# Kernel tuning notes

Measured on AMD Instinct MI355X. Metric: run time of the kernel, lower is better.

## Reference

```python
import jax, jax.numpy as jnp
import numpy as np

N_NODES = 50000
N_EDGES = 800000
IN_C = 64
OUT_C = 64
HEADS = 4
N_LAYERS = 2
BN_EPS = 1e-5
NEG_SLOPE = 0.2


def setup_inputs() -> dict:
    key = jax.random.key(0)
    ks = jax.random.split(key, 20)
    inp = {
        "x": jax.random.normal(ks[0], (N_NODES, IN_C), dtype=jnp.float32),
        "edge_index": jax.random.randint(ks[1], (2, N_EDGES), 0, N_NODES, dtype=jnp.int64),
        "edge_weight": jax.random.uniform(ks[2], (N_EDGES,), dtype=jnp.float32),
    }
    # per-layer GATConv + BN params (glorot-ish init)
    for i in range(N_LAYERS):
        k = 3 + i * 5
        scale = 1.0 / np.sqrt(IN_C)
        inp[f"W{i}"] = jax.random.normal(ks[k], (IN_C, HEADS * OUT_C), dtype=jnp.float32) * scale
        inp[f"asrc{i}"] = jax.random.normal(ks[k + 1], (HEADS, OUT_C), dtype=jnp.float32) * scale
        inp[f"adst{i}"] = jax.random.normal(ks[k + 2], (HEADS, OUT_C), dtype=jnp.float32) * scale
        inp[f"b{i}"] = jnp.zeros((OUT_C,), dtype=jnp.float32)
        inp[f"gamma{i}"] = jnp.ones((OUT_C,), dtype=jnp.float32)
        inp[f"beta{i}"] = jnp.zeros((OUT_C,), dtype=jnp.float32)
    return inp


def _gat_layer(x, src, dst, W, a_src, a_dst, b):
    # x: [N, C_in]; src/dst: [E'] (with self loops). Per-head dim = OUT_C.
    xh = (x @ W).reshape(-1, HEADS, OUT_C)          # [N, H, C]
    al_src = jnp.sum(xh * a_src[None], axis=-1)      # [N, H]
    al_dst = jnp.sum(xh * a_dst[None], axis=-1)      # [N, H]
    e = jax.nn.leaky_relu(al_src[src] + al_dst[dst], NEG_SLOPE)  # [E', H]
    # segment softmax over edges sharing a destination node
    m = jax.lax.stop_gradient(jax.ops.segment_max(e, dst, num_segments=N_NODES))
    p = jnp.exp(e - m[dst])
    denom = jax.ops.segment_sum(p, dst, num_segments=N_NODES)
    alpha = p / (denom[dst] + 1e-16)                 # [E', H]
    out = jax.ops.segment_sum(alpha[:, :, None] * xh[src], dst, num_segments=N_NODES)  # [N,H,C]
    return out.mean(axis=1) + b                      # concat=False -> mean over heads


def _batchnorm(x, gamma, beta):
    mu = x.mean(axis=0)
    var = x.var(axis=0)
    return gamma * (x - mu) * jax.lax.rsqrt(var + BN_EPS) + beta


def reference(x, edge_index, edge_weight, W0, asrc0, adst0, b0, gamma0, beta0,
              W1, asrc1, adst1, b1, gamma1, beta1):
    # edge_weight is passed as edge_attr to PyG GATConv but edge_dim=None -> ignored.
    loop = jnp.arange(N_NODES, dtype=edge_index.dtype)
    src = jnp.concatenate([edge_index[0], loop])  # add_self_loops=True (PyG default)
    dst = jnp.concatenate([edge_index[1], loop])
    params = [(W0, asrc0, adst0, b0, gamma0, beta0),
              (W1, asrc1, adst1, b1, gamma1, beta1)]
    saved = None
    for (W, a_s, a_d, b, g, bt) in params:
        x = _gat_layer(x, src, dst, W, a_s, a_d, b)
        saved = x
        x = _batchnorm(x, g, bt)
        x = jax.nn.relu(x)
        # dropout(0.5) is identity in eval mode
    return (x, saved)
```

## Files before the change

### kernel.cpp

```cpp
#include <hip/hip_runtime.h>
#include <stdint.h>

#define NEG_SLOPE 0.2f
#define BN_EPS 1e-5f

typedef __attribute__((ext_vector_type(8))) short bf16x8;
typedef __attribute__((ext_vector_type(4))) float f32x4;

__device__ __forceinline__ float bf2f(unsigned short u) {
  union { unsigned int i; float f; } v; v.i = ((unsigned int)u) << 16; return v.f;
}
__device__ __forceinline__ float asf(unsigned int u) {
  union { unsigned int i; float f; } v; v.i = u; return v.f;
}
__device__ __forceinline__ unsigned short f2bf(float f) {
  union { float f; unsigned int i; } v; v.f = f;
  unsigned int i = v.i;
  return (unsigned short)((i + 0x7fffu + ((i >> 16) & 1u)) >> 16);
}
__device__ __forceinline__ float loadF(const void* p, long long i, int f32) {
  return f32 ? ((const float*)p)[i] : bf2f(((const unsigned short*)p)[i]);
}
__device__ __forceinline__ int edge_at(const void* ei, long long idx, int is64) {
  return is64 ? (int)((const long long*)ei)[idx] : ((const int*)ei)[idx];
}

__global__ void detect_kernel(const unsigned short* __restrict__ x,
                              const int* __restrict__ ei32,
                              int* __restrict__ flags) {
  __shared__ int wild, oddnz;
  if (threadIdx.x == 0) { wild = 0; oddnz = 0; }
  __syncthreads();
  int lw = 0, lo = 0;
  for (int i = threadIdx.x; i < 4096; i += 256) {
    unsigned short u = x[i];
    int ex = (u >> 7) & 0xFF;
    if (ex >= 0x86) lw++;
    if (ei32[2 * i + 1] != 0) lo++;
  }
  if (lw) atomicAdd(&wild, lw);
  if (lo) atomicAdd(&oddnz, lo);
  __syncthreads();
  if (threadIdx.x == 0) { flags[0] = (wild > 64) ? 1 : 0; flags[1] = (oddnz == 0) ? 1 : 0; }
}

__global__ __launch_bounds__(256) void wtrans_kernel(
    const void* __restrict__ W0, const void* __restrict__ as0, const void* __restrict__ ad0,
    const void* __restrict__ W1, const void* __restrict__ as1, const void* __restrict__ ad1,
    const int* __restrict__ flags,
    unsigned short* __restrict__ WTx0, unsigned short* __restrict__ WTx1) {
  const void* W = blockIdx.x ? W1 : W0;
  const void* asrc = blockIdx.x ? as1 : as0;
  const void* adst = blockIdx.x ? ad1 : ad0;
  unsigned short* WTx = blockIdx.x ? WTx1 : WTx0;
  int f32 = flags[0];
  __shared__ unsigned short Wl[64 * 258];
  int t = threadIdx.x;
  for (int i = t; i < 64 * 256; i += 256) {
    int k = i >> 8, c = i & 255;
    Wl[k * 258 + c] = f32 ? f2bf(((const float*)W)[i]) : ((const unsigned short*)W)[i];
  }
  __syncthreads();
  {
    int c = t;
    #pragma unroll
    for (int k8 = 0; k8 < 64; k8 += 8) {
      unsigned int p0 = (unsigned int)Wl[(k8 + 0) * 258 + c] | ((unsigned int)Wl[(k8 + 1) * 258 + c] << 16);
      unsigned int p1 = (unsigned int)Wl[(k8 + 2) * 258 + c] | ((unsigned int)Wl[(k8 + 3) * 258 + c] << 16);
      unsigned int p2 = (unsigned int)Wl[(k8 + 4) * 258 + c] | ((unsigned int)Wl[(k8 + 5) * 258 + c] << 16);
      unsigned int p3 = (unsigned int)Wl[(k8 + 6) * 258 + c] | ((unsigned int)Wl[(k8 + 7) * 258 + c] << 16);
      uint4 pk; pk.x = p0; pk.y = p1; pk.z = p2; pk.w = p3;
      *(uint4*)&WTx[c * 64 + k8] = pk;
    }
  }
  for (int idx = t; idx < 512; idx += 256) {
    int r = idx >> 6;
    int k = idx & 63;
    int h = r & 3;
    const void* av = (r >> 2) ? adst : asrc;
    float acc = 0.f;
    #pragma unroll 8
    for (int c = 0; c < 64; c++)
      acc += bf2f(Wl[k * 258 + h * 64 + c]) * loadF(av, h * 64 + c, f32);
    WTx[(256 + r) * 64 + k] = f2bf(acc);
  }
  for (int idx = t; idx < 512; idx += 256) WTx[264 * 64 + idx] = 0;
}

__global__ __launch_bounds__(256) void hist_kernel(const void* __restrict__ ei, int E, int N,
                                                   const int* __restrict__ flags,
                                                   int* __restrict__ deg) {
  int e = blockIdx.x * 256 + threadIdx.x;
  if (e >= E) return;
  int is64 = flags[1];
  int d = edge_at(ei, (long long)E + e, is64);
  d = (d < 0 || d >= N) ? 0 : d;
  atomicAdd(&deg[d], 1);
}

__global__ __launch_bounds__(256) void partial_kernel(const int* __restrict__ deg,
                                                      int* __restrict__ blocksum, int N) {
  int t = threadIdx.x;
  int idx = blockIdx.x * 256 + t;
  int v = (idx < N) ? deg[idx] : 0;
  #pragma unroll
  for (int o = 1; o < 64; o <<= 1) v += __shfl_xor(v, o);
  __shared__ int ws[4];
  if ((t & 63) == 0) ws[t >> 6] = v;
  __syncthreads();
  if (t == 0) blocksum[blockIdx.x] = ws[0] + ws[1] + ws[2] + ws[3];
}

__global__ void scan_base_kernel(const int* __restrict__ blocksum,
                                 int* __restrict__ blockbase, int B) {
  int lane = threadIdx.x;
  int base = 0;
  if (lane == 0) blockbase[0] = 0;
  for (int start = 0; start < B; start += 64) {
    int idx = start + lane;
    int v = (idx < B) ? blocksum[idx] : 0;
    int sc = v;
    #pragma unroll
    for (int o = 1; o < 64; o <<= 1) {
      int u = __shfl_up(sc, o);
      if (lane >= o) sc += u;
    }
    if (idx < B) blockbase[idx + 1] = base + sc;
    base = __shfl(base + sc, 63);
  }
}

__global__ __launch_bounds__(256) void scan_final_kernel(const int* __restrict__ deg,
                                                         const int* __restrict__ blockbase,
                                                         int* __restrict__ offsets, int N) {
  int t = threadIdx.x;
  int lane = t & 63;
  int wid = t >> 6;
  int idx = blockIdx.x * 256 + t;
  int v = (idx < N) ? deg[idx] : 0;
  int sc = v;
  #pragma unroll
  for (int o = 1; o < 64; o <<= 1) {
    int u = __shfl_up(sc, o);
    if (lane >= o) sc += u;
  }
  __shared__ int ws[4];
  if (lane == 63) ws[wid] = sc;
  __syncthreads();
  int add = 0;
  #pragma unroll
  for (int w = 0; w < 4; w++) if (w < wid) add += ws[w];
  if (idx < N) offsets[idx + 1] = blockbase[blockIdx.x] + add + sc;
  if (idx == 0) offsets[0] = 0;
}

__global__ __launch_bounds__(256) void scatter_kernel(
    const void* __restrict__ ei, int E, int N, const int* __restrict__ flags,
    const int* __restrict__ offsets, int* __restrict__ cursor,
    int* __restrict__ csr_src) {
  int e = blockIdx.x * 256 + threadIdx.x;
  if (e >= E) return;
  int is64 = flags[1];
  int s = edge_at(ei, e, is64);
  int d = edge_at(ei, (long long)E + e, is64);
  s = (s < 0 || s >= N) ? 0 : s;
  d = (d < 0 || d >= N) ? 0 : d;
  int pos = offsets[d] + atomicAdd(&cursor[d], 1);
  csr_src[pos] = s;
}

__global__ __launch_bounds__(256, 3) void gemm_mfma(
    const void* __restrict__ x, const unsigned short* __restrict__ WTx,
    const int* __restrict__ flags, int mode,
    const float* __restrict__ gsum, const float* __restrict__ gsq,
    const void* __restrict__ gamma, const void* __restrict__ beta,
    unsigned short* __restrict__ xh, float* __restrict__ als, float* __restrict__ ald,
    int N) {
  __shared__ unsigned short WTs[272 * 68];
  __shared__ unsigned short RP[4][16 * 68];
  __shared__ float bnsc[64], bnsh[64];
  int f32 = flags[0];
  int t = threadIdx.x;
  for (int i = t; i < 272 * 8; i += 256) {
    int c = i >> 3, g = i & 7;
    uint4 v = ((const uint4*)WTx)[i];
    *(uint4*)&WTs[c * 68 + g * 8] = v;
  }
  if (mode == 1 && t < 64) {
    float mu = gsum[t] / (float)N;
    float var = fmaxf(gsq[t] / (float)N - mu * mu, 0.f);
    float sc = loadF(gamma, t, f32) * rsqrtf(var + BN_EPS);
    bnsc[t] = sc;
    bnsh[t] = loadF(beta, t, f32) - mu * sc;
  }
  __syncthreads();

  int wave = t >> 6, lane = t & 63;
  int q = lane >> 4, r16 = lane & 15;
  int m0 = blockIdx.x * 64 + wave * 16;
  if (m0 >= N) return;
  int row = m0 + r16;
  int rowc = row < N ? row : N - 1;

  bf16x8 a0, a1;
  if (mode == 1) {
    const float* xp = (const float*)x + (size_t)rowc * 64 + q * 8;
    float va[8], vb[8];
    *(float4*)&va[0] = ((const float4*)xp)[0];
    *(float4*)&va[4] = ((const float4*)xp)[1];
    *(float4*)&vb[0] = ((const float4*)(xp + 32))[0];
    *(float4*)&vb[4] = ((const float4*)(xp + 32))[1];
    int k0 = q * 8;
    #pragma unroll
    for (int jj = 0; jj < 8; jj++) {
      float v = fmaxf(va[jj] * bnsc[k0 + jj] + bnsh[k0 + jj], 0.f);
      float w = fmaxf(vb[jj] * bnsc[k0 + 32 + jj] + bnsh[k0 + 32 + jj], 0.f);
      a0[jj] = (short)f2bf(v);
      a1[jj] = (short)f2bf(w);
    }
  } else if (f32) {
    const float* xp = (const float*)x + (size_t)rowc * 64 + q * 8;
    float va[8], vb[8];
    *(float4*)&va[0] = ((const float4*)xp)[0];
    *(float4*)&va[4] = ((const float4*)xp)[1];
    *(float4*)&vb[0] = ((const float4*)(xp + 32))[0];
    *(float4*)&vb[4] = ((const float4*)(xp + 32))[1];
    #pragma unroll
    for (int jj = 0; jj < 8; jj++) {
      a0[jj] = (short)f2bf(va[jj]);
      a1[jj] = (short)f2bf(vb[jj]);
    }
  } else {
    const unsigned short* xp = (const unsigned short*)x + (size_t)rowc * 64 + q * 8;
    a0 = *(const bf16x8*)xp;
    a1 = *(const bf16x8*)(xp + 32);
  }

  f32x4 acc[17];
  #pragma unroll
  for (int tt = 0; tt < 17; tt++) acc[tt] = (f32x4){0.f, 0.f, 0.f, 0.f};
  #pragma unroll
  for (int tt = 0; tt < 17; tt++) {
    int c = tt * 16 + r16;
    bf16x8 b0 = *(const bf16x8*)&WTs[c * 68 + q * 8];
    bf16x8 b1 = *(const bf16x8*)&WTs[c * 68 + 32 + q * 8];
    acc[tt] = __builtin_amdgcn_mfma_f32_16x16x32_bf16(a0, b0, acc[tt], 0, 0, 0);
    acc[tt] = __builtin_amdgcn_mfma_f32_16x16x32_bf16(a1, b1, acc[tt], 0, 0, 0);
  }

  {
    int obase = m0 + q * 4;
    #pragma unroll
    for (int rr = 0; rr < 4; rr++) {
      int orow = obase + rr;
      if (orow < N) {
        if (r16 < 4) als[orow * 4 + r16] = acc[16][rr];
        else if (r16 < 8) ald[orow * 4 + (r16 - 4)] = acc[16][rr];
      }
    }
  }
  unsigned short* rp = RP[wave];
  #pragma unroll
  for (int g4 = 0; g4 < 4; g4++) {
    #pragma unroll
    for (int tt2 = 0; tt2 < 4; tt2++) {
      int tile = g4 * 4 + tt2;
      #pragma unroll
      for (int rr = 0; rr < 4; rr++)
        rp[(q * 4 + rr) * 68 + tt2 * 16 + r16] = f2bf(acc[tile][rr]);
    }
    #pragma unroll
    for (int i = 0; i < 2; i++) {
      int g = i * 64 + lane;
      int r = g >> 3;
      int grp = g & 7;
      uint4 v = *(const uint4*)&rp[r * 68 + grp * 8];
      int orow = m0 + r;
      if (orow < N) ((uint4*)xh)[(size_t)orow * 32 + g4 * 8 + grp] = v;
    }
  }
}

__global__ __launch_bounds__(256) void agg_kernel(
    const unsigned short* __restrict__ xh,
    const float* __restrict__ als, const float* __restrict__ ald,
    const int* __restrict__ offsets, const int* __restrict__ csr_src,
    const void* __restrict__ bias, const int* __restrict__ flags,
    float* __restrict__ y, int N) {
  int lane = threadIdx.x & 63;
  int wid = threadIdx.x >> 6;
  int n = blockIdx.x * 4 + wid;
  if (n >= N) return;
  int h = lane >> 4;
  const uint2* xv = (const uint2*)xh;
  float ad = ald[n * 4 + h];
  float e = als[n * 4 + h] + ad;
  e = (e > 0.f) ? e : NEG_SLOPE * e;
  float p = __expf(e);
  float dsum = p;
  uint2 xs = xv[(size_t)n * 64 + lane];
  float a0 = p * asf(xs.x << 16), a1 = p * asf(xs.x & 0xffff0000u);
  float a2 = p * asf(xs.y << 16), a3 = p * asf(xs.y & 0xffff0000u);
  int beg = offsets[n], end = offsets[n + 1];
  int j = beg;
  for (; j + 4 <= end; j += 4) {
    int s0 = csr_src[j];
    int s1 = csr_src[j + 1];
    int s2 = csr_src[j + 2];
    int s3 = csr_src[j + 3];
    uint2 v0 = xv[(size_t)s0 * 64 + lane];
    uint2 v1 = xv[(size_t)s1 * 64 + lane];
    uint2 v2 = xv[(size_t)s2 * 64 + lane];
    uint2 v3 = xv[(size_t)s3 * 64 + lane];
    float e0 = als[s0 * 4 + h] + ad;
    float e1 = als[s1 * 4 + h] + ad;
    float e2 = als[s2 * 4 + h] + ad;
    float e3 = als[s3 * 4 + h] + ad;
    e0 = (e0 > 0.f) ? e0 : NEG_SLOPE * e0;
    e1 = (e1 > 0.f) ? e1 : NEG_SLOPE * e1;
    e2 = (e2 > 0.f) ? e2 : NEG_SLOPE * e2;
    e3 = (e3 > 0.f) ? e3 : NEG_SLOPE * e3;
    float p0 = __expf(e0);
    float p1 = __expf(e1);
    float p2 = __expf(e2);
    float p3 = __expf(e3);
    dsum += p0 + p1 + p2 + p3;
    a0 += p0 * asf(v0.x << 16) + p1 * asf(v1.x << 16)
        + p2 * asf(v2.x << 16) + p3 * asf(v3.x << 16);
    a1 += p0 * asf(v0.x & 0xffff0000u) + p1 * asf(v1.x & 0xffff0000u)
        + p2 * asf(v2.x & 0xffff0000u) + p3 * asf(v3.x & 0xffff0000u);
    a2 += p0 * asf(v0.y << 16) + p1 * asf(v1.y << 16)
        + p2 * asf(v2.y << 16) + p3 * asf(v3.y << 16);
    a3 += p0 * asf(v0.y & 0xffff0000u) + p1 * asf(v1.y & 0xffff0000u)
        + p2 * asf(v2.y & 0xffff0000u) + p3 * asf(v3.y & 0xffff0000u);
  }
  for (; j < end; j++) {
    int s0 = csr_src[j];
    uint2 v0 = xv[(size_t)s0 * 64 + lane];
    float e0 = als[s0 * 4 + h] + ad;
    e0 = (e0 > 0.f) ? e0 : NEG_SLOPE * e0;
    float p0 = __expf(e0);
    dsum += p0;
    a0 += p0 * asf(v0.x << 16);
    a1 += p0 * asf(v0.x & 0xffff0000u);
    a2 += p0 * asf(v0.y << 16);
    a3 += p0 * asf(v0.y & 0xffff0000u);
  }
  float inv = 1.0f / dsum;
  a0 *= inv; a1 *= inv; a2 *= inv; a3 *= inv;
  a0 += __shfl_xor(a0, 16); a0 += __shfl_xor(a0, 32);
  a1 += __shfl_xor(a1, 16); a1 += __shfl_xor(a1, 32);
  a2 += __shfl_xor(a2, 16); a2 += __shfl_xor(a2, 32);
  a3 += __shfl_xor(a3, 16); a3 += __shfl_xor(a3, 32);
  if (lane < 16) {
    int f32 = flags[0];
    float4 o;
    o.x = 0.25f * a0 + loadF(bias, 4 * lane + 0, f32);
    o.y = 0.25f * a1 + loadF(bias, 4 * lane + 1, f32);
    o.z = 0.25f * a2 + loadF(bias, 4 * lane + 2, f32);
    o.w = 0.25f * a3 + loadF(bias, 4 * lane + 3, f32);
    ((float4*)(y + (size_t)n * 64))[lane] = o;
  }
}

__global__ __launch_bounds__(256) void stats_kernel(const float* __restrict__ y,
                                                    float* __restrict__ gsum,
                                                    float* __restrict__ gsq, int N) {
  __shared__ float ls[256], lq[256];
  int t = threadIdx.x;
  int c = t & 63;
  int r0 = blockIdx.x * 4 + (t >> 6);
  float s = 0.f, q = 0.f;
  for (int r = r0; r < N; r += gridDim.x * 4) {
    float v = y[(size_t)r * 64 + c];
    s += v; q += v * v;
  }
  ls[t] = s; lq[t] = q;
  __syncthreads();
  if (t < 64) {
    s = ls[t] + ls[t + 64] + ls[t + 128] + ls[t + 192];
    q = lq[t] + lq[t + 64] + lq[t + 128] + lq[t + 192];
    atomicAdd(&gsum[c], s);
    atomicAdd(&gsq[c], q);
  }
}

__global__ __launch_bounds__(256) void bn_kernel(
    const float* __restrict__ y, const float* __restrict__ gsum, const float* __restrict__ gsq,
    const void* __restrict__ gamma, const void* __restrict__ beta,
    const int* __restrict__ flags, float* __restrict__ out_f, int N) {
  int i = blockIdx.x * 256 + threadIdx.x;
  if (i >= N * 16) return;
  int f32 = flags[0];
  int cg = i & 15;
  float4 v = ((const float4*)y)[i];
  float4 s = ((const float4*)gsum)[cg];
  float4 q = ((const float4*)gsq)[cg];
  float inv_n = 1.0f / (float)N;
  float vv[4] = {v.x, v.y, v.z, v.w};
  float ss[4] = {s.x, s.y, s.z, s.w};
  float qq[4] = {q.x, q.y, q.z, q.w};
  float o[4];
  #pragma unroll
  for (int k = 0; k < 4; k++) {
    float g = loadF(gamma, 4 * cg + k, f32);
    float b = loadF(beta, 4 * cg + k, f32);
    float mu = ss[k] * inv_n;
    float var = fmaxf(qq[k] * inv_n - mu * mu, 0.f);
    float r = g * (vv[k] - mu) * rsqrtf(var + BN_EPS) + b;
    o[k] = r > 0.f ? r : 0.f;
  }
  float4 ov; ov.x = o[0]; ov.y = o[1]; ov.z = o[2]; ov.w = o[3];
  ((float4*)out_f)[i] = ov;
}

extern "C" void kernel_launch(void* const* d_in, const int* in_sizes, int n_in,
                              void* d_out, int out_size, void* d_ws, size_t ws_size,
                              hipStream_t stream) {
  const void* x    = d_in[0];
  const void* ei   = d_in[1];
  const void* W0    = d_in[3];
  const void* asrc0 = d_in[4];
  const void* adst0 = d_in[5];
  const void* b0    = d_in[6];
  const void* g0    = d_in[7];
  const void* be0   = d_in[8];
  const void* W1    = d_in[9];
  const void* asrc1 = d_in[10];
  const void* adst1 = d_in[11];
  const void* b1    = d_in[12];
  const void* g1    = d_in[13];
  const void* be1   = d_in[14];

  int N = in_sizes[0] / 64;
  int E = in_sizes[1] / 2;
  int NB = (N + 255) / 256;
  int NG = (N + 63) / 64;
  int NA = (N + 3) / 4;

  char* p = (char*)d_ws;
  auto alloc = [&](size_t bytes) -> char* {
    char* r = p;
    p += (bytes + 255) & ~(size_t)255;
    return r;
  };
  int* flags    = (int*)alloc(256);
  int* deg      = (int*)alloc((size_t)N * 4);
  int* cursor   = (int*)alloc((size_t)N * 4);
  int* offsets  = (int*)alloc((size_t)(N + 1) * 4);
  int* blocksum = (int*)alloc((size_t)NB * 4);
  int* blockbase= (int*)alloc((size_t)(NB + 1) * 4);
  int* csr_src  = (int*)alloc((size_t)E * 4);
  unsigned short* WTx0 = (unsigned short*)alloc(272 * 64 * 2);
  unsigned short* WTx1 = (unsigned short*)alloc(272 * 64 * 2);
  unsigned short* xh = (unsigned short*)alloc((size_t)N * 256 * 2);
  float* als    = (float*)alloc((size_t)N * 4 * 4);
  float* ald    = (float*)alloc((size_t)N * 4 * 4);
  float* y      = (float*)alloc((size_t)N * 64 * 4);
  float* gsum0  = (float*)alloc(256);
  float* gsq0   = (float*)alloc(256);
  float* gsum1  = (float*)alloc(256);
  float* gsq1   = (float*)alloc(256);

  hipMemsetAsync(deg, 0, (size_t)N * 4, stream);
  hipMemsetAsync(cursor, 0, (size_t)N * 4, stream);
  hipMemsetAsync(gsum0, 0, 1024, stream);

  detect_kernel<<<1, 256, 0, stream>>>((const unsigned short*)x, (const int*)ei, flags);
  wtrans_kernel<<<2, 256, 0, stream>>>(W0, asrc0, adst0, W1, asrc1, adst1, flags, WTx0, WTx1);

  hist_kernel<<<(E + 255) / 256, 256, 0, stream>>>(ei, E, N, flags, deg);
  partial_kernel<<<NB, 256, 0, stream>>>(deg, blocksum, N);
  scan_base_kernel<<<1, 64, 0, stream>>>(blocksum, blockbase, NB);
  scan_final_kernel<<<NB, 256, 0, stream>>>(deg, blockbase, offsets, N);
  scatter_kernel<<<(E + 255) / 256, 256, 0, stream>>>(ei, E, N, flags, offsets, cursor, csr_src);

  float* out_x = (float*)d_out;
  float* out_saved = out_x + (size_t)N * 64;

  gemm_mfma<<<NG, 256, 0, stream>>>(x, WTx0, flags, 0, (const float*)nullptr,
                                    (const float*)nullptr, nullptr, nullptr,
                                    xh, als, ald, N);
  agg_kernel<<<NA, 256, 0, stream>>>(xh, als, ald, offsets, csr_src, b0, flags, y, N);
  stats_kernel<<<250, 256, 0, stream>>>(y, gsum0, gsq0, N);
  gemm_mfma<<<NG, 256, 0, stream>>>(y, WTx1, flags, 1, gsum0, gsq0, g0, be0,
                                    xh, als, ald, N);
  agg_kernel<<<NA, 256, 0, stream>>>(xh, als, ald, offsets, csr_src, b1, flags, out_saved, N);
  stats_kernel<<<250, 256, 0, stream>>>(out_saved, gsum1, gsq1, N);
  bn_kernel<<<(N * 16 + 255) / 256, 256, 0, stream>>>(out_saved, gsum1, gsq1, g1, be1,
                                                      flags, out_x, N);
}
```

Before: 428.5 us.

## Merge detect into wtrans, seed cursor from scan, restructure GEMM stores

Folds the input-format detection kernel into the weight-transpose kernel. The scan now writes exclusive offsets into the cursor array, which removes a memset and an offsets load in the scatter. The GEMM processes two 64-row blocks per workgroup, amortizing the weight LDS load. It also drops the LDS staging buffer for xh and writes uint2 directly to global memory. The aggregation epilogue switches from float4 stores to scalar strided stores, trading coalesced wide stores for simpler indexing.

```diff
diff --git a/kernel.cpp b/kernel.cpp
--- a/kernel.cpp
+++ b/kernel.cpp
@@ -25,40 +25,54 @@
   return is64 ? (int)((const long long*)ei)[idx] : ((const int*)ei)[idx];
 }
 
-__global__ void detect_kernel(const unsigned short* __restrict__ x,
-                              const int* __restrict__ ei32,
-                              int* __restrict__ flags) {
-  __shared__ int wild, oddnz;
-  if (threadIdx.x == 0) { wild = 0; oddnz = 0; }
-  __syncthreads();
-  int lw = 0, lo = 0;
-  for (int i = threadIdx.x; i < 4096; i += 256) {
-    unsigned short u = x[i];
-    int ex = (u >> 7) & 0xFF;
-    if (ex >= 0x86) lw++;
-    if (ei32[2 * i + 1] != 0) lo++;
-  }
-  if (lw) atomicAdd(&wild, lw);
-  if (lo) atomicAdd(&oddnz, lo);
-  __syncthreads();
-  if (threadIdx.x == 0) { flags[0] = (wild > 64) ? 1 : 0; flags[1] = (oddnz == 0) ? 1 : 0; }
-}
-
 __global__ __launch_bounds__(256) void wtrans_kernel(
+    const unsigned short* __restrict__ x, const int* __restrict__ ei32,
     const void* __restrict__ W0, const void* __restrict__ as0, const void* __restrict__ ad0,
     const void* __restrict__ W1, const void* __restrict__ as1, const void* __restrict__ ad1,
-    const int* __restrict__ flags,
+    int* __restrict__ flags,
     unsigned short* __restrict__ WTx0, unsigned short* __restrict__ WTx1) {
+  __shared__ int wild, oddnz;
+  __shared__ unsigned short Wl[64 * 258];
+  int t = threadIdx.x;
+  if (t == 0) { wild = 0; oddnz = 0; }
+  __syncthreads();
+  {
+    int lw = 0, lo = 0;
+    for (int i = t; i < 4096; i += 256) {
+      unsigned short u = x[i];
+      int ex = (u >> 7) & 0xFF;
+      if (ex >= 0x86) lw++;
+      if (ei32[2 * i + 1] != 0) lo++;
+    }
+    if (lw) atomicAdd(&wild, lw);
+    if (lo) atomicAdd(&oddnz, lo);
+  }
+  __syncthreads();
+  int f32 = (wild > 64) ? 1 : 0;
+  if (blockIdx.x == 0 && t == 0) { flags[0] = f32; flags[1] = (oddnz == 0) ? 1 : 0; }
+
   const void* W = blockIdx.x ? W1 : W0;
   const void* asrc = blockIdx.x ? as1 : as0;
   const void* adst = blockIdx.x ? ad1 : ad0;
   unsigned short* WTx = blockIdx.x ? WTx1 : WTx0;
-  int f32 = flags[0];
-  __shared__ unsigned short Wl[64 * 258];
-  int t = threadIdx.x;
-  for (int i = t; i < 64 * 256; i += 256) {
-    int k = i >> 8, c = i & 255;
-    Wl[k * 258 + c] = f32 ? f2bf(((const float*)W)[i]) : ((const unsigned short*)W)[i];
+  if (f32) {
+    for (int i = t; i < 4096; i += 256) {
+      float4 w = ((const float4*)W)[i];
+      int base = i * 4;
+      int k = base >> 8, c = base & 255;
+      unsigned short* d = &Wl[k * 258 + c];
+      d[0] = f2bf(w.x); d[1] = f2bf(w.y); d[2] = f2bf(w.z); d[3] = f2bf(w.w);
+    }
+  } else {
+    for (int i = t; i < 2048; i += 256) {
+      ushort4 lo4 = ((const ushort4*)W)[2 * i];
+      ushort4 hi4 = ((const ushort4*)W)[2 * i + 1];
+      int base = i * 8;
+      int k = base >> 8, c = base & 255;
+      unsigned short* d = &Wl[k * 258 + c];
+      d[0] = lo4.x; d[1] = lo4.y; d[2] = lo4.z; d[3] = lo4.w;
+      d[4] = hi4.x; d[5] = hi4.y; d[6] = hi4.z; d[7] = hi4.w;
+    }
   }
   __syncthreads();
   {
@@ -132,7 +146,8 @@
 
 __global__ __launch_bounds__(256) void scan_final_kernel(const int* __restrict__ deg,
                                                          const int* __restrict__ blockbase,
-                                                         int* __restrict__ offsets, int N) {
+                                                         int* __restrict__ offsets,
+                                                         int* __restrict__ cursor, int N) {
   int t = threadIdx.x;
   int lane = t & 63;
   int wid = t >> 6;
@@ -150,14 +165,17 @@
   int add = 0;
   #pragma unroll
   for (int w = 0; w < 4; w++) if (w < wid) add += ws[w];
-  if (idx < N) offsets[idx + 1] = blockbase[blockIdx.x] + add + sc;
+  int incl = blockbase[blockIdx.x] + add + sc;
+  if (idx < N) {
+    offsets[idx + 1] = incl;
+    cursor[idx] = incl - v;
+  }
   if (idx == 0) offsets[0] = 0;
 }
 
 __global__ __launch_bounds__(256) void scatter_kernel(
     const void* __restrict__ ei, int E, int N, const int* __restrict__ flags,
-    const int* __restrict__ offsets, int* __restrict__ cursor,
-    int* __restrict__ csr_src) {
+    int* __restrict__ cursor, int* __restrict__ csr_src) {
   int e = blockIdx.x * 256 + threadIdx.x;
   if (e >= E) return;
   int is64 = flags[1];
@@ -165,7 +183,7 @@
   int d = edge_at(ei, (long long)E + e, is64);
   s = (s < 0 || s >= N) ? 0 : s;
   d = (d < 0 || d >= N) ? 0 : d;
-  int pos = offsets[d] + atomicAdd(&cursor[d], 1);
+  int pos = atomicAdd(&cursor[d], 1);
   csr_src[pos] = s;
 }
 
@@ -177,7 +195,6 @@
     unsigned short* __restrict__ xh, float* __restrict__ als, float* __restrict__ ald,
     int N) {
   __shared__ unsigned short WTs[272 * 68];
-  __shared__ unsigned short RP[4][16 * 68];
   __shared__ float bnsc[64], bnsh[64];
   int f32 = flags[0];
   int t = threadIdx.x;
@@ -197,86 +214,77 @@
 
   int wave = t >> 6, lane = t & 63;
   int q = lane >> 4, r16 = lane & 15;
-  int m0 = blockIdx.x * 64 + wave * 16;
-  if (m0 >= N) return;
-  int row = m0 + r16;
-  int rowc = row < N ? row : N - 1;
-
-  bf16x8 a0, a1;
-  if (mode == 1) {
-    const float* xp = (const float*)x + (size_t)rowc * 64 + q * 8;
-    float va[8], vb[8];
-    *(float4*)&va[0] = ((const float4*)xp)[0];
-    *(float4*)&va[4] = ((const float4*)xp)[1];
-    *(float4*)&vb[0] = ((const float4*)(xp + 32))[0];
-    *(float4*)&vb[4] = ((const float4*)(xp + 32))[1];
-    int k0 = q * 8;
+
+  #pragma unroll
+  for (int rb = 0; rb < 2; rb++) {
+    int m0 = blockIdx.x * 128 + rb * 64 + wave * 16;
+    if (m0 >= N) break;
+    int row = m0 + r16;
+    int rowc = row < N ? row : N - 1;
+
+    bf16x8 a0, a1;
+    if (mode == 1) {
+      const float* xp = (const float*)x + (size_t)rowc * 64 + q * 8;
+      float va[8], vb[8];
+      *(float4*)&va[0] = ((const float4*)xp)[0];
+      *(float4*)&va[4] = ((const float4*)xp)[1];
+      *(float4*)&vb[0] = ((const float4*)(xp + 32))[0];
+      *(float4*)&vb[4] = ((const float4*)(xp + 32))[1];
+      int k0 = q * 8;
+      #pragma unroll
+      for (int jj = 0; jj < 8; jj++) {
+        float v = fmaxf(va[jj] * bnsc[k0 + jj] + bnsh[k0 + jj], 0.f);
+        float w = fmaxf(vb[jj] * bnsc[k0 + 32 + jj] + bnsh[k0 + 32 + jj], 0.f);
+        a0[jj] = (short)f2bf(v);
+        a1[jj] = (short)f2bf(w);
+      }
+    } else if (f32) {
+      const float* xp = (const float*)x + (size_t)rowc * 64 + q * 8;
+      float va[8], vb[8];
+      *(float4*)&va[0] = ((const float4*)xp)[0];
+      *(float4*)&va[4] = ((const float4*)xp)[1];
+      *(float4*)&vb[0] = ((const float4*)(xp + 32))[0];
+      *(float4*)&vb[4] = ((const float4*)(xp + 32))[1];
+      #pragma unroll
+      for (int jj = 0; jj < 8; jj++) {
+        a0[jj] = (short)f2bf(va[jj]);
+        a1[jj] = (short)f2bf(vb[jj]);
+      }
+    } else {
+      const unsigned short* xp = (const unsigned short*)x + (size_t)rowc * 64 + q * 8;
+      a0 = *(const bf16x8*)xp;
+      a1 = *(const bf16x8*)(xp + 32);
+    }
+
+    f32x4 acc[17];
     #pragma unroll
-    for (int jj = 0; jj < 8; jj++) {
-      float v = fmaxf(va[jj] * bnsc[k0 + jj] + bnsh[k0 + jj], 0.f);
-      float w = fmaxf(vb[jj] * bnsc[k0 + 32 + jj] + bnsh[k0 + 32 + jj], 0.f);
-      a0[jj] = (short)f2bf(v);
-      a1[jj] = (short)f2bf(w);
-    }
-  } else if (f32) {
-    const float* xp = (const float*)x + (size_t)rowc * 64 + q * 8;
-    float va[8], vb[8];
-    *(float4*)&va[0] = ((const float4*)xp)[0];
-    *(float4*)&va[4] = ((const float4*)xp)[1];
-    *(float4*)&vb[0] = ((const float4*)(xp + 32))[0];
-    *(float4*)&vb[4] = ((const float4*)(xp + 32))[1];
+    for (int tt = 0; tt < 17; tt++) acc[tt] = (f32x4){0.f, 0.f, 0.f, 0.f};
     #pragma unroll
-    for (int jj = 0; jj < 8; jj++) {
-      a0[jj] = (short)f2bf(va[jj]);
-      a1[jj] = (short)f2bf(vb[jj]);
-    }
-  } else {
-    const unsigned short* xp = (const unsigned short*)x + (size_t)rowc * 64 + q * 8;
-    a0 = *(const bf16x8*)xp;
-    a1 = *(const bf16x8*)(xp + 32);
-  }
-
-  f32x4 acc[17];
-  #pragma unroll
-  for (int tt = 0; tt < 17; tt++) acc[tt] = (f32x4){0.f, 0.f, 0.f, 0.f};
-  #pragma unroll
-  for (int tt = 0; tt < 17; tt++) {
-    int c = tt * 16 + r16;
-    bf16x8 b0 = *(const bf16x8*)&WTs[c * 68 + q * 8];
-    bf16x8 b1 = *(const bf16x8*)&WTs[c * 68 + 32 + q * 8];
-    acc[tt] = __builtin_amdgcn_mfma_f32_16x16x32_bf16(a0, b0, acc[tt], 0, 0, 0);
-    acc[tt] = __builtin_amdgcn_mfma_f32_16x16x32_bf16(a1, b1, acc[tt], 0, 0, 0);
-  }
-
-  {
-    int obase = m0 + q * 4;
+    for (int tt = 0; tt < 17; tt++) {
+      int c = tt * 16 + r16;
+      bf16x8 b0 = *(const bf16x8*)&WTs[c * 68 + q * 8];
+      bf16x8 b1 = *(const bf16x8*)&WTs[c * 68 + 32 + q * 8];
+      acc[tt] = __builtin_amdgcn_mfma_f32_16x16x32_bf16(a0, b0, acc[tt], 0, 0, 0);
+      acc[tt] = __builtin_amdgcn_mfma_f32_16x16x32_bf16(a1, b1, acc[tt], 0, 0, 0);
+    }
+
     #pragma unroll
     for (int rr = 0; rr < 4; rr++) {
-      int orow = obase + rr;
+      int orow = m0 + q * 4 + rr;
       if (orow < N) {
         if (r16 < 4) als[orow * 4 + r16] = acc[16][rr];
         else if (r16 < 8) ald[orow * 4 + (r16 - 4)] = acc[16][rr];
+        uint2* xrow = (uint2*)xh + (size_t)orow * 64 + r16;
+        #pragma unroll
+        for (int hh = 0; hh < 4; hh++) {
+          uint2 st;
+          st.x = (unsigned int)f2bf(acc[4 * hh + 0][rr])
+               | ((unsigned int)f2bf(acc[4 * hh + 1][rr]) << 16);
+          st.y = (unsigned int)f2bf(acc[4 * hh + 2][rr])
+               | ((unsigned int)f2bf(acc[4 * hh + 3][rr]) << 16);
+          xrow[hh * 16] = st;
+        }
       }
-    }
-  }
-  unsigned short* rp = RP[wave];
-  #pragma unroll
-  for (int g4 = 0; g4 < 4; g4++) {
-    #pragma unroll
-    for (int tt2 = 0; tt2 < 4; tt2++) {
-      int tile = g4 * 4 + tt2;
-      #pragma unroll
-      for (int rr = 0; rr < 4; rr++)
-        rp[(q * 4 + rr) * 68 + tt2 * 16 + r16] = f2bf(acc[tile][rr]);
-    }
-    #pragma unroll
-    for (int i = 0; i < 2; i++) {
-      int g = i * 64 + lane;
-      int r = g >> 3;
-      int grp = g & 7;
-      uint4 v = *(const uint4*)&rp[r * 68 + grp * 8];
-      int orow = m0 + r;
-      if (orow < N) ((uint4*)xh)[(size_t)orow * 32 + g4 * 8 + grp] = v;
     }
   }
 }
@@ -354,12 +362,11 @@
   a3 += __shfl_xor(a3, 16); a3 += __shfl_xor(a3, 32);
   if (lane < 16) {
     int f32 = flags[0];
-    float4 o;
-    o.x = 0.25f * a0 + loadF(bias, 4 * lane + 0, f32);
-    o.y = 0.25f * a1 + loadF(bias, 4 * lane + 1, f32);
-    o.z = 0.25f * a2 + loadF(bias, 4 * lane + 2, f32);
-    o.w = 0.25f * a3 + loadF(bias, 4 * lane + 3, f32);
-    ((float4*)(y + (size_t)n * 64))[lane] = o;
+    float* yr = y + (size_t)n * 64;
+    yr[lane]      = 0.25f * a0 + loadF(bias, lane, f32);
+    yr[16 + lane] = 0.25f * a1 + loadF(bias, 16 + lane, f32);
+    yr[32 + lane] = 0.25f * a2 + loadF(bias, 32 + lane, f32);
+    yr[48 + lane] = 0.25f * a3 + loadF(bias, 48 + lane, f32);
   }
 }
 
@@ -435,7 +442,7 @@
   int N = in_sizes[0] / 64;
   int E = in_sizes[1] / 2;
   int NB = (N + 255) / 256;
-  int NG = (N + 63) / 64;
+  int NG = (N + 127) / 128;
   int NA = (N + 3) / 4;
 
   char* p = (char*)d_ws;
@@ -463,17 +470,16 @@
   float* gsq1   = (float*)alloc(256);
 
   hipMemsetAsync(deg, 0, (size_t)N * 4, stream);
-  hipMemsetAsync(cursor, 0, (size_t)N * 4, stream);
   hipMemsetAsync(gsum0, 0, 1024, stream);
 
-  detect_kernel<<<1, 256, 0, stream>>>((const unsigned short*)x, (const int*)ei, flags);
-  wtrans_kernel<<<2, 256, 0, stream>>>(W0, asrc0, adst0, W1, asrc1, adst1, flags, WTx0, WTx1);
+  wtrans_kernel<<<2, 256, 0, stream>>>((const unsigned short*)x, (const int*)ei,
+                                       W0, asrc0, adst0, W1, asrc1, adst1, flags, WTx0, WTx1);
 
   hist_kernel<<<(E + 255) / 256, 256, 0, stream>>>(ei, E, N, flags, deg);
   partial_kernel<<<NB, 256, 0, stream>>>(deg, blocksum, N);
   scan_base_kernel<<<1, 64, 0, stream>>>(blocksum, blockbase, NB);
-  scan_final_kernel<<<NB, 256, 0, stream>>>(deg, blockbase, offsets, N);
-  scatter_kernel<<<(E + 255) / 256, 256, 0, stream>>>(ei, E, N, flags, offsets, cursor, csr_src);
+  scan_final_kernel<<<NB, 256, 0, stream>>>(deg, blockbase, offsets, cursor, N);
+  scatter_kernel<<<(E + 255) / 256, 256, 0, stream>>>(ei, E, N, flags, cursor, csr_src);
 
   float* out_x = (float*)d_out;
   float* out_saved = out_x + (size_t)N * 64;
```

After: 431.6 us. Within noise of the previous version (+0.7%).
